# Kernel optimization log

Hardware: AMD Instinct MI355X
Metric: run time of the kernel (lower is better)

Reference implementation:

```python
import jax, jax.numpy as jnp
import numpy as np

N_GROUPS = 8
N_TOPK_GROUP = 4
TOPK = 8
ROUTED_SCALE = 2.5


def setup_inputs() -> dict:
    key = jax.random.key(0)
    k1, k2, k3 = jax.random.split(key, 3)
    T, D, E = 8192, 7168, 256
    x = jax.random.normal(k1, (T, D), dtype=jnp.float32)
    weight = jax.random.normal(k2, (E, D), dtype=jnp.float32) * 0.02
    bias = jax.random.normal(k3, (E,), dtype=jnp.float32) * 0.02
    return {"x": x, "weight": weight, "bias": bias}


def reference(x, weight, bias):
    T = x.shape[0]
    # gate projection + sigmoid -> routing scores [T, E]
    scores = jax.nn.sigmoid(jnp.einsum("td,ed->te", x, weight))
    original_scores = scores
    s = scores + bias
    # grouped top-k routing: [T, G, E/G]
    sg = s.reshape(T, N_GROUPS, -1)
    # group score = sum of top-2 expert scores within each group
    group_scores = jax.lax.top_k(sg, 2)[0].sum(axis=-1)        # [T, G]
    _, gidx = jax.lax.top_k(group_scores, N_TOPK_GROUP)        # [T, n_topk_group]
    keep = jnp.zeros((T, N_GROUPS), dtype=bool)
    keep = keep.at[jnp.arange(T)[:, None], gidx].set(True)
    sg = jnp.where(keep[:, :, None], sg, -jnp.inf)
    s = sg.reshape(T, -1)
    # per-token top-k experts over surviving groups
    _, indices = jax.lax.top_k(s, TOPK)                        # [T, topk]
    weights = jnp.take_along_axis(original_scores, indices, axis=1)
    weights = weights / weights.sum(axis=-1, keepdims=True) * ROUTED_SCALE
    return weights.astype(x.dtype), indices
```

## Files before the change

### kernel.cpp

```cpp
#include <hip/hip_runtime.h>
#include <hip/hip_bf16.h>
#include <math.h>


typedef _Float16 f16x8 __attribute__((ext_vector_type(8)));
typedef float    f32x4 __attribute__((ext_vector_type(4)));

__device__ __forceinline__ void glds16(const void* g, void* l) {
  __builtin_amdgcn_global_load_lds(
      (const __attribute__((address_space(1))) void*)g,
      (__attribute__((address_space(3))) void*)l, 16, 0, 0);
}

__device__ __forceinline__ unsigned short f2h(float f) {
  _Float16 h = (_Float16)f;
  return __builtin_bit_cast(unsigned short, h);
}
__device__ __forceinline__ float h2f(unsigned short b) {
  return (float)__builtin_bit_cast(_Float16, b);
}

__device__ __forceinline__ int swz(int gi, int row) {
  return gi ^ (row & 3) ^ ((row >> 2) & 3);
}

__global__ __launch_bounds__(256) void convert_w(
    const float* __restrict__ W,
    unsigned short* __restrict__ Whi, unsigned short* __restrict__ Wlo)
{
  const int e = blockIdx.x;
  const int t = threadIdx.x;
  if (t >= 224) return;
  const int r = e & 127, bn = e >> 7;
  const float* src = W + (size_t)e * 7168 + t * 32;
  const size_t tbase = (size_t)(bn * 224 + t) * 4096 + (size_t)r * 32;
  #pragma unroll
  for (int g = 0; g < 4; ++g) {
    unsigned int hw[4], lw[4];
    #pragma unroll
    for (int p = 0; p < 4; ++p) {
      float f0 = src[g * 8 + 2 * p] * 64.0f;
      float f1 = src[g * 8 + 2 * p + 1] * 64.0f;
      unsigned short h0 = f2h(f0), h1 = f2h(f1);
      unsigned short l0 = f2h((f0 - h2f(h0)) * 2048.0f);
      unsigned short l1 = f2h((f1 - h2f(h1)) * 2048.0f);
      hw[p] = (unsigned)h0 | ((unsigned)h1 << 16);
      lw[p] = (unsigned)l0 | ((unsigned)l1 << 16);
    }
    const size_t base = tbase + (size_t)(swz(g, r) * 8);
    *(uint4*)(Whi + base) = make_uint4(hw[0], hw[1], hw[2], hw[3]);
    *(uint4*)(Wlo + base) = make_uint4(lw[0], lw[1], lw[2], lw[3]);
  }
}

__global__ __launch_bounds__(256, 2) void gate_gemm(
    const float* __restrict__ X,
    const unsigned short* __restrict__ Whi,
    const unsigned short* __restrict__ Wlo,
    float* __restrict__ Spart, int D, int TILES, int KS)
{
  __shared__ char lds[65536];

  const int bid = blockIdx.x;
  const int ks = bid % KS;
  const int bn = (bid / KS) & 1;
  const int bm = bid / (2 * KS);
  const int tid = threadIdx.x, lane = tid & 63, wid = tid >> 6;
  const int wm = wid >> 1, wn = wid & 1;
  const int TM = bm * 128;
  const int k0base = ks * TILES * 32;

  const int srow = tid >> 1, skq = tid & 1;
  const float* xsrc = X + (size_t)(TM + srow) * D + k0base + skq * 16;
  const int aw0 = srow * 64 + swz(skq * 2 + 0, srow) * 16;
  const int aw1 = srow * 64 + swz(skq * 2 + 1, srow) * 16;

  const unsigned short* wh_tile = Whi + (size_t)(bn * 224 + ks * TILES) * 4096;
  const unsigned short* wl_tile = Wlo + (size_t)(bn * 224 + ks * TILES) * 4096;

  f32x4 acc1[4][4], acc2[4][4];
  #pragma unroll
  for (int m = 0; m < 4; ++m)
    #pragma unroll
    for (int n = 0; n < 4; ++n) { acc1[m][n] = (f32x4)0.0f; acc2[m][n] = (f32x4)0.0f; }

  int aro[4], bro[4];
  const int gi = lane >> 4;
  #pragma unroll
  for (int m = 0; m < 4; ++m) {
    const int row = wm * 64 + m * 16 + (lane & 15);
    aro[m] = row * 64 + swz(gi, row) * 16;
  }
  #pragma unroll
  for (int n = 0; n < 4; ++n) {
    const int row = wn * 64 + n * 16 + (lane & 15);
    bro[n] = row * 64 + swz(gi, row) * 16;
  }

  float4 pa[4], pb[4];
  {
    #pragma unroll
    for (int i = 0; i < 2; ++i) {
      const int c = wid * 2 + i;
      glds16(wh_tile + c * 512 + lane * 8, lds + 16384 + c * 1024);
      glds16(wl_tile + c * 512 + lane * 8, lds + 24576 + c * 1024);
    }
    __builtin_amdgcn_sched_barrier(0);
    float4 a[4];
    #pragma unroll
    for (int i = 0; i < 4; ++i) a[i] = *(const float4*)(xsrc + i * 4);
    unsigned int hw[8], lw[8];
    #pragma unroll
    for (int q = 0; q < 8; ++q) {
      float f0 = ((const float*)a)[2 * q], f1 = ((const float*)a)[2 * q + 1];
      unsigned short h0 = f2h(f0), h1 = f2h(f1);
      unsigned short l0 = f2h((f0 - h2f(h0)) * 2048.0f);
      unsigned short l1 = f2h((f1 - h2f(h1)) * 2048.0f);
      hw[q] = (unsigned)h0 | ((unsigned)h1 << 16);
      lw[q] = (unsigned)l0 | ((unsigned)l1 << 16);
    }
    *(uint4*)(lds + aw0)        = make_uint4(hw[0], hw[1], hw[2], hw[3]);
    *(uint4*)(lds + aw1)        = make_uint4(hw[4], hw[5], hw[6], hw[7]);
    *(uint4*)(lds + 8192 + aw0) = make_uint4(lw[0], lw[1], lw[2], lw[3]);
    *(uint4*)(lds + 8192 + aw1) = make_uint4(lw[4], lw[5], lw[6], lw[7]);
    const int s1 = (TILES > 1) ? 1 : 0;
    #pragma unroll
    for (int i = 0; i < 4; ++i)
      pa[i] = *(const float4*)(xsrc + (size_t)s1 * 32 + i * 4);
    __builtin_amdgcn_sched_barrier(0);
  }
  asm volatile("s_waitcnt vmcnt(4) lgkmcnt(0)" ::: "memory");
  __builtin_amdgcn_sched_barrier(0);
  __builtin_amdgcn_s_barrier();

  int cur = 0;
  for (int s = 0; s < TILES; ++s) {
    const int nxt = cur ^ 1;
    char* base_c = lds + cur * 32768;
    char* base_n = lds + nxt * 32768;
    const bool stage_next = (s + 1 < TILES);

    if (stage_next) {
      const unsigned short* wh = wh_tile + (size_t)(s + 1) * 4096;
      const unsigned short* wl = wl_tile + (size_t)(s + 1) * 4096;
      #pragma unroll
      for (int i = 0; i < 2; ++i) {
        const int c = wid * 2 + i;
        glds16(wh + c * 512 + lane * 8, base_n + 16384 + c * 1024);
        glds16(wl + c * 512 + lane * 8, base_n + 24576 + c * 1024);
      }
    }
    __builtin_amdgcn_sched_barrier(0);

    {
      int sn = s + 2; if (sn > TILES - 1) sn = TILES - 1;
      #pragma unroll
      for (int i = 0; i < 4; ++i)
        pb[i] = *(const float4*)(xsrc + (size_t)sn * 32 + i * 4);
    }
    __builtin_amdgcn_sched_barrier(0);

    {
      const char* Ahi = base_c;          const char* Alo = base_c + 8192;
      const char* Bh  = base_c + 16384;  const char* Bl  = base_c + 24576;
      f16x8 ah[4], al[4], bh[4], bl[4];
      #pragma unroll
      for (int m = 0; m < 4; ++m) {
        ah[m] = *(const f16x8*)(Ahi + aro[m]);
        al[m] = *(const f16x8*)(Alo + aro[m]);
      }
      #pragma unroll
      for (int n = 0; n < 4; ++n) {
        bh[n] = *(const f16x8*)(Bh + bro[n]);
        bl[n] = *(const f16x8*)(Bl + bro[n]);
      }
      __builtin_amdgcn_s_setprio(1);
      #pragma unroll
      for (int m = 0; m < 4; ++m)
        #pragma unroll
        for (int n = 0; n < 4; ++n) {
          acc1[m][n] = __builtin_amdgcn_mfma_f32_16x16x32_f16(ah[m], bh[n], acc1[m][n], 0, 0, 0);
          acc2[m][n] = __builtin_amdgcn_mfma_f32_16x16x32_f16(ah[m], bl[n], acc2[m][n], 0, 0, 0);
          acc2[m][n] = __builtin_amdgcn_mfma_f32_16x16x32_f16(al[m], bh[n], acc2[m][n], 0, 0, 0);
        }
      __builtin_amdgcn_s_setprio(0);
    }

    if (stage_next) {
      unsigned int hw[8], lw[8];
      #pragma unroll
      for (int q = 0; q < 8; ++q) {
        float f0 = ((const float*)pa)[2 * q], f1 = ((const float*)pa)[2 * q + 1];
        unsigned short h0 = f2h(f0), h1 = f2h(f1);
        unsigned short l0 = f2h((f0 - h2f(h0)) * 2048.0f);
        unsigned short l1 = f2h((f1 - h2f(h1)) * 2048.0f);
        hw[q] = (unsigned)h0 | ((unsigned)h1 << 16);
        lw[q] = (unsigned)l0 | ((unsigned)l1 << 16);
      }
      *(uint4*)(base_n + aw0)        = make_uint4(hw[0], hw[1], hw[2], hw[3]);
      *(uint4*)(base_n + aw1)        = make_uint4(hw[4], hw[5], hw[6], hw[7]);
      *(uint4*)(base_n + 8192 + aw0) = make_uint4(lw[0], lw[1], lw[2], lw[3]);
      *(uint4*)(base_n + 8192 + aw1) = make_uint4(lw[4], lw[5], lw[6], lw[7]);
    }
    #pragma unroll
    for (int i = 0; i < 4; ++i) pa[i] = pb[i];

    asm volatile("s_waitcnt vmcnt(4) lgkmcnt(0)" ::: "memory");
    __builtin_amdgcn_sched_barrier(0);
    __builtin_amdgcn_s_barrier();

    cur = nxt;
  }

  float* Sp = Spart + (size_t)ks * 8192 * 256;
  #pragma unroll
  for (int m = 0; m < 4; ++m)
    #pragma unroll
    for (int n = 0; n < 4; ++n)
      #pragma unroll
      for (int r = 0; r < 4; ++r) {
        const int t = TM + wm * 64 + m * 16 + (lane >> 4) * 4 + r;
        const int e = bn * 128 + wn * 64 + n * 16 + (lane & 15);
        Sp[(size_t)t * 256 + e] =
            (acc1[m][n][r] + acc2[m][n][r] * (1.0f / 2048.0f)) * (1.0f / 64.0f);
      }
}

__global__ __launch_bounds__(256) void gate_routing(
    const float* __restrict__ Spart, int KS,
    const float* __restrict__ bias,
    float* __restrict__ outw, float* __restrict__ outi, int T)
{
  const int lane = threadIdx.x & 63;
  const int wave = threadIdx.x >> 6;
  const int t = blockIdx.x * 4 + wave;
  if (t >= T) return;

  double l[4] = {0.0, 0.0, 0.0, 0.0};
  for (int ks = 0; ks < KS; ++ks) {
    float4 p = *(const float4*)(Spart + (size_t)ks * T * 256
                                + (size_t)t * 256 + lane * 4);
    l[0] += (double)p.x; l[1] += (double)p.y;
    l[2] += (double)p.z; l[3] += (double)p.w;
  }

  float4 bi = *(const float4*)(bias + lane * 4);
  float orig[4], s[4];
  #pragma unroll
  for (int u = 0; u < 4; ++u)
    orig[u] = 1.0f / (1.0f + expf(-(float)l[u]));
  s[0] = orig[0] + bi.x; s[1] = orig[1] + bi.y;
  s[2] = orig[2] + bi.z; s[3] = orig[3] + bi.w;

  float m1 = -INFINITY, m2 = -INFINITY;
  #pragma unroll
  for (int u = 0; u < 4; ++u) {
    float v = s[u];
    if (v > m1) { m2 = m1; m1 = v; }
    else if (v > m2) { m2 = v; }
  }
  #pragma unroll
  for (int off = 1; off < 8; off <<= 1) {
    float o1 = __shfl_xor(m1, off, 64);
    float o2 = __shfl_xor(m2, off, 64);
    if (o1 > m1) { m2 = fmaxf(m1, o2); m1 = o1; }
    else         { m2 = fmaxf(m2, o1); }
  }
  const float gscore = m1 + m2;

  const int g = lane >> 3;
  int rank = 0;
  #pragma unroll
  for (int j = 0; j < 8; ++j) {
    float gs = __shfl(gscore, j * 8, 64);
    rank += (gs > gscore || (gs == gscore && j < g)) ? 1 : 0;
  }
  if (rank >= 4) { s[0] = s[1] = s[2] = s[3] = -INFINITY; }

  float wsum = 0.0f, sel_w = 0.0f;
  int sel_i = 0;
  #pragma unroll
  for (int it = 0; it < 8; ++it) {
    float bv = s[0]; int bu = 0;
    #pragma unroll
    for (int u = 1; u < 4; ++u)
      if (s[u] > bv) { bv = s[u]; bu = u; }
    float v = bv;
    int ix = lane * 4 + bu;
    float og = orig[bu];
    #pragma unroll
    for (int off = 1; off < 64; off <<= 1) {
      float ov  = __shfl_xor(v,  off, 64);
      int   oix = __shfl_xor(ix, off, 64);
      float oog = __shfl_xor(og, off, 64);
      if (ov > v || (ov == v && oix < ix)) { v = ov; ix = oix; og = oog; }
    }
    if (lane == it) { sel_w = og; sel_i = ix; }
    wsum += og;
    if ((ix >> 2) == lane) s[ix & 3] = -INFINITY;
  }

  if (lane < 8) {
    outw[(size_t)t * 8 + lane] = sel_w / wsum * 2.5f;
    outi[(size_t)t * 8 + lane] = (float)sel_i;
  }
}

extern "C" void kernel_launch(void* const* d_in, const int* in_sizes, int n_in,
                              void* d_out, int out_size, void* d_ws, size_t ws_size,
                              hipStream_t stream) {
  const float* x = (const float*)d_in[0];
  const float* w = (const float*)d_in[1];
  const float* b = (const float*)d_in[2];
  const int E = in_sizes[2];
  const int D = in_sizes[1] / E;
  const int T = in_sizes[0] / D;

  unsigned short* Whi = (unsigned short*)d_ws;
  unsigned short* Wlo = (unsigned short*)((char*)d_ws + (4u << 20));
  float* Spart = (float*)((char*)d_ws + (8u << 20));

  const size_t per_part = (size_t)T * E * 4;
  int KS = 2;
  if (ws_size >= (8u << 20) + 8 * per_part) KS = 8;
  else if (ws_size >= (8u << 20) + 4 * per_part) KS = 4;
  const int TILES = D / (32 * KS);

  float* outw = (float*)d_out;
  float* outi = outw + (size_t)T * 8;

  convert_w<<<E, 256, 0, stream>>>(w, Whi, Wlo);
  gate_gemm<<<2 * KS * (T / 128), 256, 0, stream>>>(x, Whi, Wlo, Spart, D, TILES, KS);
  gate_routing<<<(T + 3) / 4, 256, 0, stream>>>(Spart, KS, b, outw, outi, T);
}
```

Measured before the change: 147.4 us.

## Split main loop into four sub-phases interleaving loads, staging and MFMA

Restructures each K-tile iteration into four phases, one per N sub-block. Each phase loads one B fragment, issues part of the global prefetch or the fp32-to-split-fp16 staging, then runs that sub-block's MFMAs. The aim is to spread memory and conversion work between MFMA bursts, ping-pong style, so latency is hidden better. In exchange it adds two workgroup barriers per phase (eight per tile instead of one), which may add synchronisation overhead.

After: 155.2 us. 1.05x slower.

```diff
diff --git a/kernel.cpp b/kernel.cpp
--- a/kernel.cpp
+++ b/kernel.cpp
@@ -135,81 +135,86 @@
 
   int cur = 0;
   for (int s = 0; s < TILES; ++s) {
-    const int nxt = cur ^ 1;
     char* base_c = lds + cur * 32768;
-    char* base_n = lds + nxt * 32768;
+    char* base_n = lds + (cur ^ 1) * 32768;
     const bool stage_next = (s + 1 < TILES);
 
-    if (stage_next) {
-      const unsigned short* wh = wh_tile + (size_t)(s + 1) * 4096;
-      const unsigned short* wl = wl_tile + (size_t)(s + 1) * 4096;
-      #pragma unroll
-      for (int i = 0; i < 2; ++i) {
-        const int c = wid * 2 + i;
-        glds16(wh + c * 512 + lane * 8, base_n + 16384 + c * 1024);
-        glds16(wl + c * 512 + lane * 8, base_n + 24576 + c * 1024);
-      }
-    }
-    __builtin_amdgcn_sched_barrier(0);
-
-    {
-      int sn = s + 2; if (sn > TILES - 1) sn = TILES - 1;
-      #pragma unroll
-      for (int i = 0; i < 4; ++i)
-        pb[i] = *(const float4*)(xsrc + (size_t)sn * 32 + i * 4);
-    }
-    __builtin_amdgcn_sched_barrier(0);
-
-    {
-      const char* Ahi = base_c;          const char* Alo = base_c + 8192;
-      const char* Bh  = base_c + 16384;  const char* Bl  = base_c + 24576;
-      f16x8 ah[4], al[4], bh[4], bl[4];
+    f16x8 ah[4], al[4];
+
+    #pragma unroll
+    for (int q = 0; q < 4; ++q) {
+      if (q == 0) {
+        #pragma unroll
+        for (int m = 0; m < 4; ++m) {
+          ah[m] = *(const f16x8*)(base_c + aro[m]);
+          al[m] = *(const f16x8*)(base_c + 8192 + aro[m]);
+        }
+      }
+      f16x8 bh = *(const f16x8*)(base_c + 16384 + bro[q]);
+      f16x8 bl = *(const f16x8*)(base_c + 24576 + bro[q]);
+
+      if (q == 0 && stage_next) {
+        const unsigned short* wh = wh_tile + (size_t)(s + 1) * 4096;
+        #pragma unroll
+        for (int i = 0; i < 2; ++i) {
+          const int c = wid * 2 + i;
+          glds16(wh + c * 512 + lane * 8, base_n + 16384 + c * 1024);
+        }
+      }
+      if (q == 1 && stage_next) {
+        const unsigned short* wl = wl_tile + (size_t)(s + 1) * 4096;
+        #pragma unroll
+        for (int i = 0; i < 2; ++i) {
+          const int c = wid * 2 + i;
+          glds16(wl + c * 512 + lane * 8, base_n + 24576 + c * 1024);
+        }
+      }
+      if (q == 2) {
+        __builtin_amdgcn_sched_barrier(0);
+        int sn = s + 2; if (sn > TILES - 1) sn = TILES - 1;
+        #pragma unroll
+        for (int i = 0; i < 4; ++i)
+          pb[i] = *(const float4*)(xsrc + (size_t)sn * 32 + i * 4);
+        __builtin_amdgcn_sched_barrier(0);
+      }
+      if (q == 3 && stage_next) {
+        unsigned int hw[8], lw[8];
+        #pragma unroll
+        for (int p = 0; p < 8; ++p) {
+          float f0 = ((const float*)pa)[2 * p], f1 = ((const float*)pa)[2 * p + 1];
+          unsigned short h0 = f2h(f0), h1 = f2h(f1);
+          unsigned short l0 = f2h((f0 - h2f(h0)) * 2048.0f);
+          unsigned short l1 = f2h((f1 - h2f(h1)) * 2048.0f);
+          hw[p] = (unsigned)h0 | ((unsigned)h1 << 16);
+          lw[p] = (unsigned)l0 | ((unsigned)l1 << 16);
+        }
+        *(uint4*)(base_n + aw0)        = make_uint4(hw[0], hw[1], hw[2], hw[3]);
+        *(uint4*)(base_n + aw1)        = make_uint4(hw[4], hw[5], hw[6], hw[7]);
+        *(uint4*)(base_n + 8192 + aw0) = make_uint4(lw[0], lw[1], lw[2], lw[3]);
+        *(uint4*)(base_n + 8192 + aw1) = make_uint4(lw[4], lw[5], lw[6], lw[7]);
+      }
+
+      __builtin_amdgcn_s_barrier();
+      asm volatile("s_waitcnt lgkmcnt(0)" ::: "memory");
+      __builtin_amdgcn_sched_barrier(0);
+      __builtin_amdgcn_s_setprio(1);
       #pragma unroll
       for (int m = 0; m < 4; ++m) {
-        ah[m] = *(const f16x8*)(Ahi + aro[m]);
-        al[m] = *(const f16x8*)(Alo + aro[m]);
-      }
-      #pragma unroll
-      for (int n = 0; n < 4; ++n) {
-        bh[n] = *(const f16x8*)(Bh + bro[n]);
-        bl[n] = *(const f16x8*)(Bl + bro[n]);
-      }
-      __builtin_amdgcn_s_setprio(1);
-      #pragma unroll
-      for (int m = 0; m < 4; ++m)
-        #pragma unroll
-        for (int n = 0; n < 4; ++n) {
-          acc1[m][n] = __builtin_amdgcn_mfma_f32_16x16x32_f16(ah[m], bh[n], acc1[m][n], 0, 0, 0);
-          acc2[m][n] = __builtin_amdgcn_mfma_f32_16x16x32_f16(ah[m], bl[n], acc2[m][n], 0, 0, 0);
-          acc2[m][n] = __builtin_amdgcn_mfma_f32_16x16x32_f16(al[m], bh[n], acc2[m][n], 0, 0, 0);
-        }
+        acc1[m][q] = __builtin_amdgcn_mfma_f32_16x16x32_f16(ah[m], bh, acc1[m][q], 0, 0, 0);
+        acc2[m][q] = __builtin_amdgcn_mfma_f32_16x16x32_f16(ah[m], bl, acc2[m][q], 0, 0, 0);
+        acc2[m][q] = __builtin_amdgcn_mfma_f32_16x16x32_f16(al[m], bh, acc2[m][q], 0, 0, 0);
+      }
       __builtin_amdgcn_s_setprio(0);
-    }
-
-    if (stage_next) {
-      unsigned int hw[8], lw[8];
-      #pragma unroll
-      for (int q = 0; q < 8; ++q) {
-        float f0 = ((const float*)pa)[2 * q], f1 = ((const float*)pa)[2 * q + 1];
-        unsigned short h0 = f2h(f0), h1 = f2h(f1);
-        unsigned short l0 = f2h((f0 - h2f(h0)) * 2048.0f);
-        unsigned short l1 = f2h((f1 - h2f(h1)) * 2048.0f);
-        hw[q] = (unsigned)h0 | ((unsigned)h1 << 16);
-        lw[q] = (unsigned)l0 | ((unsigned)l1 << 16);
-      }
-      *(uint4*)(base_n + aw0)        = make_uint4(hw[0], hw[1], hw[2], hw[3]);
-      *(uint4*)(base_n + aw1)        = make_uint4(hw[4], hw[5], hw[6], hw[7]);
-      *(uint4*)(base_n + 8192 + aw0) = make_uint4(lw[0], lw[1], lw[2], lw[3]);
-      *(uint4*)(base_n + 8192 + aw1) = make_uint4(lw[4], lw[5], lw[6], lw[7]);
-    }
+      if (q == 3) {
+        asm volatile("s_waitcnt vmcnt(4)" ::: "memory");
+        __builtin_amdgcn_sched_barrier(0);
+      }
+      __builtin_amdgcn_s_barrier();
+    }
+
     #pragma unroll
     for (int i = 0; i < 4; ++i) pa[i] = pb[i];
-
-    asm volatile("s_waitcnt vmcnt(4) lgkmcnt(0)" ::: "memory");
-    __builtin_amdgcn_sched_barrier(0);
-    __builtin_amdgcn_s_barrier();
-
-    cur = nxt;
+    cur ^= 1;
   }
 
   float* Sp = Spart + (size_t)ks * 8192 * 256;
```

## Split split-fp16 GEMM into hi-hi and cross-term passes with 256x256 tiles

Applied to the files above, without the earlier changes.

The fused three-MFMA gate GEMM becomes two launches of a templated kernel. The first computes only the hi*hi product, and the second computes the two cross terms and read-modify-writes them into the partial sums. Tiles grow to 256 tokens by all 256 experts with 512 threads, so the weight layout is rearranged and each X tile is converted once for all experts, not twice. The cross pass needs 128KB of dynamic LDS, which may limit occupancy, and it adds a second full pass over X plus read-modify-write traffic on Spart.

Result: slower. 186.9 us (+26.8%).

```diff
diff --git a/kernel.cpp b/kernel.cpp
--- a/kernel.cpp
+++ b/kernel.cpp
@@ -31,9 +31,8 @@
   const int e = blockIdx.x;
   const int t = threadIdx.x;
   if (t >= 224) return;
-  const int r = e & 127, bn = e >> 7;
   const float* src = W + (size_t)e * 7168 + t * 32;
-  const size_t tbase = (size_t)(bn * 224 + t) * 4096 + (size_t)r * 32;
+  const size_t tbase = (size_t)t * 8192 + (size_t)e * 32;
   #pragma unroll
   for (int g = 0; g < 4; ++g) {
     unsigned int hw[4], lw[4];
@@ -47,48 +46,52 @@
       hw[p] = (unsigned)h0 | ((unsigned)h1 << 16);
       lw[p] = (unsigned)l0 | ((unsigned)l1 << 16);
     }
-    const size_t base = tbase + (size_t)(swz(g, r) * 8);
+    const size_t base = tbase + (size_t)(swz(g, e) * 8);
     *(uint4*)(Whi + base) = make_uint4(hw[0], hw[1], hw[2], hw[3]);
     *(uint4*)(Wlo + base) = make_uint4(lw[0], lw[1], lw[2], lw[3]);
   }
 }
 
-__global__ __launch_bounds__(256, 2) void gate_gemm(
+template<int CROSS>
+__global__ __launch_bounds__(512, 2) void gate_gemm(
     const float* __restrict__ X,
     const unsigned short* __restrict__ Whi,
     const unsigned short* __restrict__ Wlo,
     float* __restrict__ Spart, int D, int TILES, int KS)
 {
-  __shared__ char lds[65536];
+  extern __shared__ char lds[];
+  const int BUF   = CROSS ? 65536 : 32768;
+  const int O_ALO = 16384;
+  const int O_BH  = CROSS ? 32768 : 16384;
+  const int O_BL  = 49152;
 
   const int bid = blockIdx.x;
   const int ks = bid % KS;
-  const int bn = (bid / KS) & 1;
-  const int bm = bid / (2 * KS);
+  const int bm = bid / KS;
   const int tid = threadIdx.x, lane = tid & 63, wid = tid >> 6;
-  const int wm = wid >> 1, wn = wid & 1;
-  const int TM = bm * 128;
-  const int k0base = ks * TILES * 32;
-
-  const int srow = tid >> 1, skq = tid & 1;
-  const float* xsrc = X + (size_t)(TM + srow) * D + k0base + skq * 16;
-  const int aw0 = srow * 64 + swz(skq * 2 + 0, srow) * 16;
-  const int aw1 = srow * 64 + swz(skq * 2 + 1, srow) * 16;
-
-  const unsigned short* wh_tile = Whi + (size_t)(bn * 224 + ks * TILES) * 4096;
-  const unsigned short* wl_tile = Wlo + (size_t)(bn * 224 + ks * TILES) * 4096;
-
-  f32x4 acc1[4][4], acc2[4][4];
-  #pragma unroll
-  for (int m = 0; m < 4; ++m)
-    #pragma unroll
-    for (int n = 0; n < 4; ++n) { acc1[m][n] = (f32x4)0.0f; acc2[m][n] = (f32x4)0.0f; }
-
-  int aro[4], bro[4];
+  const int wm = wid >> 2, wn = wid & 3;
+  const int TM = bm * 256;
+  const int k0 = ks * TILES * 32;
+
+  const int srow = tid >> 1, half = tid & 1;
+  const float* xsrc = X + (size_t)(TM + srow) * D + k0 + half * 16;
+  const int aw0 = srow * 64 + swz(half * 2 + 0, srow) * 16;
+  const int aw1 = srow * 64 + swz(half * 2 + 1, srow) * 16;
+
+  const unsigned short* wh_tile = Whi + (size_t)(ks * TILES) * 8192;
+  const unsigned short* wl_tile = Wlo + (size_t)(ks * TILES) * 8192;
+
+  f32x4 acc[8][4];
+  #pragma unroll
+  for (int m = 0; m < 8; ++m)
+    #pragma unroll
+    for (int n = 0; n < 4; ++n) acc[m][n] = (f32x4)0.0f;
+
+  int aro[8], bro[4];
   const int gi = lane >> 4;
   #pragma unroll
-  for (int m = 0; m < 4; ++m) {
-    const int row = wm * 64 + m * 16 + (lane & 15);
+  for (int m = 0; m < 8; ++m) {
+    const int row = wm * 128 + m * 16 + (lane & 15);
     aro[m] = row * 64 + swz(gi, row) * 16;
   }
   #pragma unroll
@@ -98,12 +101,13 @@
   }
 
   float4 pa[4], pb[4];
+
   {
     #pragma unroll
     for (int i = 0; i < 2; ++i) {
       const int c = wid * 2 + i;
-      glds16(wh_tile + c * 512 + lane * 8, lds + 16384 + c * 1024);
-      glds16(wl_tile + c * 512 + lane * 8, lds + 24576 + c * 1024);
+      glds16(wh_tile + c * 512 + lane * 8, lds + O_BH + c * 1024);
+      if (CROSS) glds16(wl_tile + c * 512 + lane * 8, lds + O_BL + c * 1024);
     }
     __builtin_amdgcn_sched_barrier(0);
     float4 a[4];
@@ -114,15 +118,19 @@
     for (int q = 0; q < 8; ++q) {
       float f0 = ((const float*)a)[2 * q], f1 = ((const float*)a)[2 * q + 1];
       unsigned short h0 = f2h(f0), h1 = f2h(f1);
-      unsigned short l0 = f2h((f0 - h2f(h0)) * 2048.0f);
-      unsigned short l1 = f2h((f1 - h2f(h1)) * 2048.0f);
       hw[q] = (unsigned)h0 | ((unsigned)h1 << 16);
-      lw[q] = (unsigned)l0 | ((unsigned)l1 << 16);
-    }
-    *(uint4*)(lds + aw0)        = make_uint4(hw[0], hw[1], hw[2], hw[3]);
-    *(uint4*)(lds + aw1)        = make_uint4(hw[4], hw[5], hw[6], hw[7]);
-    *(uint4*)(lds + 8192 + aw0) = make_uint4(lw[0], lw[1], lw[2], lw[3]);
-    *(uint4*)(lds + 8192 + aw1) = make_uint4(lw[4], lw[5], lw[6], lw[7]);
+      if (CROSS) {
+        unsigned short l0 = f2h((f0 - h2f(h0)) * 2048.0f);
+        unsigned short l1 = f2h((f1 - h2f(h1)) * 2048.0f);
+        lw[q] = (unsigned)l0 | ((unsigned)l1 << 16);
+      }
+    }
+    *(uint4*)(lds + aw0) = make_uint4(hw[0], hw[1], hw[2], hw[3]);
+    *(uint4*)(lds + aw1) = make_uint4(hw[4], hw[5], hw[6], hw[7]);
+    if (CROSS) {
+      *(uint4*)(lds + O_ALO + aw0) = make_uint4(lw[0], lw[1], lw[2], lw[3]);
+      *(uint4*)(lds + O_ALO + aw1) = make_uint4(lw[4], lw[5], lw[6], lw[7]);
+    }
     const int s1 = (TILES > 1) ? 1 : 0;
     #pragma unroll
     for (int i = 0; i < 4; ++i)
@@ -135,19 +143,18 @@
 
   int cur = 0;
   for (int s = 0; s < TILES; ++s) {
-    const int nxt = cur ^ 1;
-    char* base_c = lds + cur * 32768;
-    char* base_n = lds + nxt * 32768;
+    char* base_c = lds + cur * BUF;
+    char* base_n = lds + (cur ^ 1) * BUF;
     const bool stage_next = (s + 1 < TILES);
 
     if (stage_next) {
-      const unsigned short* wh = wh_tile + (size_t)(s + 1) * 4096;
-      const unsigned short* wl = wl_tile + (size_t)(s + 1) * 4096;
+      const unsigned short* wh = wh_tile + (size_t)(s + 1) * 8192;
+      const unsigned short* wl = wl_tile + (size_t)(s + 1) * 8192;
       #pragma unroll
       for (int i = 0; i < 2; ++i) {
         const int c = wid * 2 + i;
-        glds16(wh + c * 512 + lane * 8, base_n + 16384 + c * 1024);
-        glds16(wl + c * 512 + lane * 8, base_n + 24576 + c * 1024);
+        glds16(wh + c * 512 + lane * 8, base_n + O_BH + c * 1024);
+        if (CROSS) glds16(wl + c * 512 + lane * 8, base_n + O_BL + c * 1024);
       }
     }
     __builtin_amdgcn_sched_barrier(0);
@@ -161,28 +168,29 @@
     __builtin_amdgcn_sched_barrier(0);
 
     {
-      const char* Ahi = base_c;          const char* Alo = base_c + 8192;
-      const char* Bh  = base_c + 16384;  const char* Bl  = base_c + 24576;
-      f16x8 ah[4], al[4], bh[4], bl[4];
-      #pragma unroll
-      for (int m = 0; m < 4; ++m) {
-        ah[m] = *(const f16x8*)(Ahi + aro[m]);
-        al[m] = *(const f16x8*)(Alo + aro[m]);
-      }
+      f16x8 bh[4], bl[4];
       #pragma unroll
       for (int n = 0; n < 4; ++n) {
-        bh[n] = *(const f16x8*)(Bh + bro[n]);
-        bl[n] = *(const f16x8*)(Bl + bro[n]);
+        bh[n] = *(const f16x8*)(base_c + O_BH + bro[n]);
+        if (CROSS) bl[n] = *(const f16x8*)(base_c + O_BL + bro[n]);
       }
       __builtin_amdgcn_s_setprio(1);
       #pragma unroll
-      for (int m = 0; m < 4; ++m)
-        #pragma unroll
-        for (int n = 0; n < 4; ++n) {
-          acc1[m][n] = __builtin_amdgcn_mfma_f32_16x16x32_f16(ah[m], bh[n], acc1[m][n], 0, 0, 0);
-          acc2[m][n] = __builtin_amdgcn_mfma_f32_16x16x32_f16(ah[m], bl[n], acc2[m][n], 0, 0, 0);
-          acc2[m][n] = __builtin_amdgcn_mfma_f32_16x16x32_f16(al[m], bh[n], acc2[m][n], 0, 0, 0);
+      for (int m = 0; m < 8; ++m) {
+        f16x8 ah = *(const f16x8*)(base_c + aro[m]);
+        if (!CROSS) {
+          #pragma unroll
+          for (int n = 0; n < 4; ++n)
+            acc[m][n] = __builtin_amdgcn_mfma_f32_16x16x32_f16(ah, bh[n], acc[m][n], 0, 0, 0);
+        } else {
+          f16x8 al = *(const f16x8*)(base_c + O_ALO + aro[m]);
+          #pragma unroll
+          for (int n = 0; n < 4; ++n) {
+            acc[m][n] = __builtin_amdgcn_mfma_f32_16x16x32_f16(ah, bl[n], acc[m][n], 0, 0, 0);
+            acc[m][n] = __builtin_amdgcn_mfma_f32_16x16x32_f16(al, bh[n], acc[m][n], 0, 0, 0);
+          }
         }
+      }
       __builtin_amdgcn_s_setprio(0);
     }
 
@@ -192,15 +200,19 @@
       for (int q = 0; q < 8; ++q) {
         float f0 = ((const float*)pa)[2 * q], f1 = ((const float*)pa)[2 * q + 1];
         unsigned short h0 = f2h(f0), h1 = f2h(f1);
-        unsigned short l0 = f2h((f0 - h2f(h0)) * 2048.0f);
-        unsigned short l1 = f2h((f1 - h2f(h1)) * 2048.0f);
         hw[q] = (unsigned)h0 | ((unsigned)h1 << 16);
-        lw[q] = (unsigned)l0 | ((unsigned)l1 << 16);
-      }
-      *(uint4*)(base_n + aw0)        = make_uint4(hw[0], hw[1], hw[2], hw[3]);
-      *(uint4*)(base_n + aw1)        = make_uint4(hw[4], hw[5], hw[6], hw[7]);
-      *(uint4*)(base_n + 8192 + aw0) = make_uint4(lw[0], lw[1], lw[2], lw[3]);
-      *(uint4*)(base_n + 8192 + aw1) = make_uint4(lw[4], lw[5], lw[6], lw[7]);
+        if (CROSS) {
+          unsigned short l0 = f2h((f0 - h2f(h0)) * 2048.0f);
+          unsigned short l1 = f2h((f1 - h2f(h1)) * 2048.0f);
+          lw[q] = (unsigned)l0 | ((unsigned)l1 << 16);
+        }
+      }
+      *(uint4*)(base_n + aw0) = make_uint4(hw[0], hw[1], hw[2], hw[3]);
+      *(uint4*)(base_n + aw1) = make_uint4(hw[4], hw[5], hw[6], hw[7]);
+      if (CROSS) {
+        *(uint4*)(base_n + O_ALO + aw0) = make_uint4(lw[0], lw[1], lw[2], lw[3]);
+        *(uint4*)(base_n + O_ALO + aw1) = make_uint4(lw[4], lw[5], lw[6], lw[7]);
+      }
     }
     #pragma unroll
     for (int i = 0; i < 4; ++i) pa[i] = pb[i];
@@ -209,20 +221,22 @@
     __builtin_amdgcn_sched_barrier(0);
     __builtin_amdgcn_s_barrier();
 
-    cur = nxt;
+    cur ^= 1;
   }
 
   float* Sp = Spart + (size_t)ks * 8192 * 256;
   #pragma unroll
-  for (int m = 0; m < 4; ++m)
+  for (int m = 0; m < 8; ++m)
     #pragma unroll
     for (int n = 0; n < 4; ++n)
       #pragma unroll
       for (int r = 0; r < 4; ++r) {
-        const int t = TM + wm * 64 + m * 16 + (lane >> 4) * 4 + r;
-        const int e = bn * 128 + wn * 64 + n * 16 + (lane & 15);
-        Sp[(size_t)t * 256 + e] =
-            (acc1[m][n][r] + acc2[m][n][r] * (1.0f / 2048.0f)) * (1.0f / 64.0f);
+        const int t = TM + wm * 128 + m * 16 + (lane >> 4) * 4 + r;
+        const int e = wn * 64 + n * 16 + (lane & 15);
+        if (CROSS)
+          Sp[(size_t)t * 256 + e] += acc[m][n][r] * (1.0f / 2048.0f);
+        else
+          Sp[(size_t)t * 256 + e] = acc[m][n][r];
       }
 }
 
@@ -248,7 +262,7 @@
   float orig[4], s[4];
   #pragma unroll
   for (int u = 0; u < 4; ++u)
-    orig[u] = 1.0f / (1.0f + expf(-(float)l[u]));
+    orig[u] = 1.0f / (1.0f + expf(-(float)(l[u] * (1.0 / 64.0))));
   s[0] = orig[0] + bi.x; s[1] = orig[1] + bi.y;
   s[2] = orig[2] + bi.z; s[3] = orig[3] + bi.w;
 
@@ -321,15 +335,16 @@
   float* Spart = (float*)((char*)d_ws + (8u << 20));
 
   const size_t per_part = (size_t)T * E * 4;
-  int KS = 2;
+  int KS = 4;
   if (ws_size >= (8u << 20) + 8 * per_part) KS = 8;
-  else if (ws_size >= (8u << 20) + 4 * per_part) KS = 4;
   const int TILES = D / (32 * KS);
 
   float* outw = (float*)d_out;
   float* outi = outw + (size_t)T * 8;
 
   convert_w<<<E, 256, 0, stream>>>(w, Whi, Wlo);
-  gate_gemm<<<2 * KS * (T / 128), 256, 0, stream>>>(x, Whi, Wlo, Spart, D, TILES, KS);
+  const int grid = (T / 256) * KS;
+  gate_gemm<0><<<grid, 512, 65536,  stream>>>(x, Whi, Wlo, Spart, D, TILES, KS);
+  gate_gemm<1><<<grid, 512, 131072, stream>>>(x, Whi, Wlo, Spart, D, TILES, KS);
   gate_routing<<<(T + 3) / 4, 256, 0, stream>>>(Spart, KS, b, outw, outi, T);
 }
```

## Screen with single-fp16 GEMM, refine only near-tie tokens in split precision

Applied to the files above, without the earlier changes.

Replaces the three-MFMA hi/lo split GEMM with a single fp16 pass over all tokens, and adds a screening kernel that flags tokens whose top-k or group selection falls within a small margin. Only the flagged tokens are recomputed with the full split-precision GEMM and routed again. The intent is to cut MFMA work and LDS traffic roughly threefold for most tokens. In exchange the kernel relies on heuristic margins being wide enough to catch every precision-sensitive selection, and it adds atomics, extra launches and a refine pass whose size depends on the data.

Result: slower. 352.4 us (+139.1%).

```diff
diff --git a/kernel.cpp b/kernel.cpp
--- a/kernel.cpp
+++ b/kernel.cpp
@@ -2,6 +2,9 @@
 #include <hip/hip_bf16.h>
 #include <math.h>
 
+
+#define MARGIN  2.0e-3f
+#define GMARGIN 4.0e-3f
 
 typedef _Float16 f16x8 __attribute__((ext_vector_type(8)));
 typedef float    f32x4 __attribute__((ext_vector_type(4)));
@@ -11,7 +14,6 @@
       (const __attribute__((address_space(1))) void*)g,
       (__attribute__((address_space(3))) void*)l, 16, 0, 0);
 }
-
 __device__ __forceinline__ unsigned short f2h(float f) {
   _Float16 h = (_Float16)f;
   return __builtin_bit_cast(unsigned short, h);
@@ -19,18 +21,18 @@
 __device__ __forceinline__ float h2f(unsigned short b) {
   return (float)__builtin_bit_cast(_Float16, b);
 }
-
 __device__ __forceinline__ int swz(int gi, int row) {
   return gi ^ (row & 3) ^ ((row >> 2) & 3);
 }
 
 __global__ __launch_bounds__(256) void convert_w(
     const float* __restrict__ W,
-    unsigned short* __restrict__ Whi, unsigned short* __restrict__ Wlo)
+    unsigned short* __restrict__ Whi, unsigned short* __restrict__ Wlo,
+    int* __restrict__ cnt)
 {
   const int e = blockIdx.x;
   const int t = threadIdx.x;
-  if (t >= 224) return;
+  if (t >= 224) { if (e == 0 && t == 224) *cnt = 0; return; }
   const int r = e & 127, bn = e >> 7;
   const float* src = W + (size_t)e * 7168 + t * 32;
   const size_t tbase = (size_t)(bn * 224 + t) * 4096 + (size_t)r * 32;
@@ -53,13 +55,12 @@
   }
 }
 
-__global__ __launch_bounds__(256, 2) void gate_gemm(
+__global__ __launch_bounds__(256, 3) void gate_gemm_approx(
     const float* __restrict__ X,
     const unsigned short* __restrict__ Whi,
-    const unsigned short* __restrict__ Wlo,
     float* __restrict__ Spart, int D, int TILES, int KS)
 {
-  __shared__ char lds[65536];
+  __shared__ char lds[32768];
 
   const int bid = blockIdx.x;
   const int ks = bid % KS;
@@ -76,13 +77,12 @@
   const int aw1 = srow * 64 + swz(skq * 2 + 1, srow) * 16;
 
   const unsigned short* wh_tile = Whi + (size_t)(bn * 224 + ks * TILES) * 4096;
-  const unsigned short* wl_tile = Wlo + (size_t)(bn * 224 + ks * TILES) * 4096;
-
-  f32x4 acc1[4][4], acc2[4][4];
+
+  f32x4 acc[4][4];
   #pragma unroll
   for (int m = 0; m < 4; ++m)
     #pragma unroll
-    for (int n = 0; n < 4; ++n) { acc1[m][n] = (f32x4)0.0f; acc2[m][n] = (f32x4)0.0f; }
+    for (int n = 0; n < 4; ++n) acc[m][n] = (f32x4)0.0f;
 
   int aro[4], bro[4];
   const int gi = lane >> 4;
@@ -102,81 +102,322 @@
     #pragma unroll
     for (int i = 0; i < 2; ++i) {
       const int c = wid * 2 + i;
-      glds16(wh_tile + c * 512 + lane * 8, lds + 16384 + c * 1024);
-      glds16(wl_tile + c * 512 + lane * 8, lds + 24576 + c * 1024);
+      glds16(wh_tile + c * 512 + lane * 8, lds + 8192 + c * 1024);
     }
     __builtin_amdgcn_sched_barrier(0);
     float4 a[4];
     #pragma unroll
     for (int i = 0; i < 4; ++i) a[i] = *(const float4*)(xsrc + i * 4);
-    unsigned int hw[8], lw[8];
+    unsigned int hw[8];
     #pragma unroll
     for (int q = 0; q < 8; ++q) {
       float f0 = ((const float*)a)[2 * q], f1 = ((const float*)a)[2 * q + 1];
+      hw[q] = (unsigned)f2h(f0) | ((unsigned)f2h(f1) << 16);
+    }
+    *(uint4*)(lds + aw0) = make_uint4(hw[0], hw[1], hw[2], hw[3]);
+    *(uint4*)(lds + aw1) = make_uint4(hw[4], hw[5], hw[6], hw[7]);
+    const int s1 = (TILES > 1) ? 1 : 0;
+    #pragma unroll
+    for (int i = 0; i < 4; ++i)
+      pa[i] = *(const float4*)(xsrc + (size_t)s1 * 32 + i * 4);
+    __builtin_amdgcn_sched_barrier(0);
+  }
+  asm volatile("s_waitcnt vmcnt(4) lgkmcnt(0)" ::: "memory");
+  __builtin_amdgcn_sched_barrier(0);
+  __builtin_amdgcn_s_barrier();
+
+  int cur = 0;
+  for (int s = 0; s < TILES; ++s) {
+    char* base_c = lds + cur * 16384;
+    char* base_n = lds + (cur ^ 1) * 16384;
+    const bool stage_next = (s + 1 < TILES);
+
+    if (stage_next) {
+      const unsigned short* wh = wh_tile + (size_t)(s + 1) * 4096;
+      #pragma unroll
+      for (int i = 0; i < 2; ++i) {
+        const int c = wid * 2 + i;
+        glds16(wh + c * 512 + lane * 8, base_n + 8192 + c * 1024);
+      }
+    }
+    __builtin_amdgcn_sched_barrier(0);
+    {
+      int sn = s + 2; if (sn > TILES - 1) sn = TILES - 1;
+      #pragma unroll
+      for (int i = 0; i < 4; ++i)
+        pb[i] = *(const float4*)(xsrc + (size_t)sn * 32 + i * 4);
+    }
+    __builtin_amdgcn_sched_barrier(0);
+    {
+      f16x8 ah[4], bh[4];
+      #pragma unroll
+      for (int m = 0; m < 4; ++m) ah[m] = *(const f16x8*)(base_c + aro[m]);
+      #pragma unroll
+      for (int n = 0; n < 4; ++n) bh[n] = *(const f16x8*)(base_c + 8192 + bro[n]);
+      __builtin_amdgcn_s_setprio(1);
+      #pragma unroll
+      for (int m = 0; m < 4; ++m)
+        #pragma unroll
+        for (int n = 0; n < 4; ++n)
+          acc[m][n] = __builtin_amdgcn_mfma_f32_16x16x32_f16(ah[m], bh[n], acc[m][n], 0, 0, 0);
+      __builtin_amdgcn_s_setprio(0);
+    }
+    if (stage_next) {
+      unsigned int hw[8];
+      #pragma unroll
+      for (int q = 0; q < 8; ++q) {
+        float f0 = ((const float*)pa)[2 * q], f1 = ((const float*)pa)[2 * q + 1];
+        hw[q] = (unsigned)f2h(f0) | ((unsigned)f2h(f1) << 16);
+      }
+      *(uint4*)(base_n + aw0) = make_uint4(hw[0], hw[1], hw[2], hw[3]);
+      *(uint4*)(base_n + aw1) = make_uint4(hw[4], hw[5], hw[6], hw[7]);
+    }
+    #pragma unroll
+    for (int i = 0; i < 4; ++i) pa[i] = pb[i];
+
+    asm volatile("s_waitcnt vmcnt(4) lgkmcnt(0)" ::: "memory");
+    __builtin_amdgcn_sched_barrier(0);
+    __builtin_amdgcn_s_barrier();
+    cur ^= 1;
+  }
+
+  float* Sp = Spart + (size_t)ks * 8192 * 256;
+  #pragma unroll
+  for (int m = 0; m < 4; ++m)
+    #pragma unroll
+    for (int n = 0; n < 4; ++n)
+      #pragma unroll
+      for (int r = 0; r < 4; ++r) {
+        const int t = TM + wm * 64 + m * 16 + (lane >> 4) * 4 + r;
+        const int e = bn * 128 + wn * 64 + n * 16 + (lane & 15);
+        Sp[(size_t)t * 256 + e] = acc[m][n][r] * (1.0f / 64.0f);
+      }
+}
+
+__global__ __launch_bounds__(256) void gate_screen(
+    const float* __restrict__ Spart, int KS,
+    const float* __restrict__ bias,
+    float* __restrict__ outw, float* __restrict__ outi, int T,
+    int* __restrict__ cnt, int* __restrict__ list)
+{
+  const int lane = threadIdx.x & 63;
+  const int wave = threadIdx.x >> 6;
+  const int t = blockIdx.x * 4 + wave;
+  if (t >= T) return;
+
+  double l[4] = {0.0, 0.0, 0.0, 0.0};
+  for (int ks = 0; ks < KS; ++ks) {
+    float4 p = *(const float4*)(Spart + (size_t)ks * T * 256
+                                + (size_t)t * 256 + lane * 4);
+    l[0] += (double)p.x; l[1] += (double)p.y;
+    l[2] += (double)p.z; l[3] += (double)p.w;
+  }
+
+  float4 bi = *(const float4*)(bias + lane * 4);
+  float orig[4], s[4];
+  #pragma unroll
+  for (int u = 0; u < 4; ++u)
+    orig[u] = 1.0f / (1.0f + expf(-(float)l[u]));
+  s[0] = orig[0] + bi.x; s[1] = orig[1] + bi.y;
+  s[2] = orig[2] + bi.z; s[3] = orig[3] + bi.w;
+
+  float m1 = -INFINITY, m2 = -INFINITY;
+  #pragma unroll
+  for (int u = 0; u < 4; ++u) {
+    float v = s[u];
+    if (v > m1) { m2 = m1; m1 = v; }
+    else if (v > m2) { m2 = v; }
+  }
+  #pragma unroll
+  for (int off = 1; off < 8; off <<= 1) {
+    float o1 = __shfl_xor(m1, off, 64);
+    float o2 = __shfl_xor(m2, off, 64);
+    if (o1 > m1) { m2 = fmaxf(m1, o2); m1 = o1; }
+    else         { m2 = fmaxf(m2, o1); }
+  }
+  const float gscore = m1 + m2;
+
+  const int g = lane >> 3;
+  int rank = 0;
+  float g4 = -INFINITY, g5 = -INFINITY;
+  #pragma unroll
+  for (int j = 0; j < 8; ++j) {
+    float gs = __shfl(gscore, j * 8, 64);
+    rank += (gs > gscore || (gs == gscore && j < g)) ? 1 : 0;
+    int rj = 0;
+    #pragma unroll
+    for (int jj = 0; jj < 8; ++jj) {
+      float gjj = __shfl(gscore, jj * 8, 64);
+      rj += (gjj > gs || (gjj == gs && jj < j)) ? 1 : 0;
+    }
+    if (rj == 3) g4 = gs;
+    if (rj == 4) g5 = gs;
+  }
+  if (rank >= 4) { s[0] = s[1] = s[2] = s[3] = -INFINITY; }
+
+  float wsum = 0.0f, sel_w = 0.0f;
+  int sel_i = 0;
+  float prev_v = 0.0f, gapmin = INFINITY;
+  for (int it = 0; it < 9; ++it) {
+    float bv = s[0]; int bu = 0;
+    #pragma unroll
+    for (int u = 1; u < 4; ++u)
+      if (s[u] > bv) { bv = s[u]; bu = u; }
+    float v = bv;
+    int ix = lane * 4 + bu;
+    float og = orig[bu];
+    #pragma unroll
+    for (int off = 1; off < 64; off <<= 1) {
+      float ov  = __shfl_xor(v,  off, 64);
+      int   oix = __shfl_xor(ix, off, 64);
+      float oog = __shfl_xor(og, off, 64);
+      if (ov > v || (ov == v && oix < ix)) { v = ov; ix = oix; og = oog; }
+    }
+    if (it > 0) gapmin = fminf(gapmin, prev_v - v);
+    prev_v = v;
+    if (it < 8) {
+      if (lane == it) { sel_w = og; sel_i = ix; }
+      wsum += og;
+      if ((ix >> 2) == lane) s[ix & 3] = -INFINITY;
+    }
+  }
+
+  if (lane < 8) {
+    outw[(size_t)t * 8 + lane] = sel_w / wsum * 2.5f;
+    outi[(size_t)t * 8 + lane] = (float)sel_i;
+  }
+
+  const bool flag = (g4 - g5 < GMARGIN) || (gapmin < MARGIN);
+  if (flag && lane == 0) {
+    int pos = atomicAdd(cnt, 1);
+    list[pos] = t;
+  }
+}
+
+__global__ __launch_bounds__(256, 2) void gate_refine_gemm(
+    const float* __restrict__ X,
+    const unsigned short* __restrict__ Whi,
+    const unsigned short* __restrict__ Wlo,
+    float* __restrict__ Rpart, int D, int TILES, int KS,
+    const int* __restrict__ cnt, const int* __restrict__ list)
+{
+  const int count = *cnt;
+  const int bid = blockIdx.x;
+  const int ks = bid % KS;
+  const int bm = bid / KS;
+  if (bm * 32 >= count) return;
+
+  __shared__ char lds[73728];
+
+  const int tid = threadIdx.x, lane = tid & 63, wid = tid >> 6;
+  const int k0base = ks * TILES * 32;
+
+  const int srow = tid >> 3, sub = tid & 7;
+  const int sgi = sub >> 1, shalf = sub & 1;
+  int slot = bm * 32 + srow;
+  int sl = slot < count ? slot : count - 1;
+  const int tok = list[sl];
+  const float* xsrc = X + (size_t)tok * D + k0base + sub * 4;
+  const int aw = srow * 64 + swz(sgi, srow) * 16 + shalf * 8;
+
+  const unsigned short* wh_t0 = Whi + (size_t)(ks * TILES) * 4096;
+  const unsigned short* wh_t1 = Whi + (size_t)(224 + ks * TILES) * 4096;
+  const unsigned short* wl_t0 = Wlo + (size_t)(ks * TILES) * 4096;
+  const unsigned short* wl_t1 = Wlo + (size_t)(224 + ks * TILES) * 4096;
+
+  f32x4 acc1[2][4], acc2[2][4];
+  #pragma unroll
+  for (int m = 0; m < 2; ++m)
+    #pragma unroll
+    for (int n = 0; n < 4; ++n) { acc1[m][n] = (f32x4)0.0f; acc2[m][n] = (f32x4)0.0f; }
+
+  int aro[2], bro[4];
+  const int gi = lane >> 4;
+  #pragma unroll
+  for (int m = 0; m < 2; ++m) {
+    const int row = m * 16 + (lane & 15);
+    aro[m] = row * 64 + swz(gi, row) * 16;
+  }
+  #pragma unroll
+  for (int n = 0; n < 4; ++n) {
+    const int row = wid * 64 + n * 16 + (lane & 15);
+    bro[n] = row * 64 + swz(gi, row) * 16;
+  }
+
+  float4 pa, pb;
+  {
+    #pragma unroll
+    for (int i = 0; i < 4; ++i) {
+      const int c = wid * 4 + i;
+      const unsigned short* sh = (c < 8) ? (wh_t0 + (c & 7) * 512)
+                                         : (wh_t1 + (c & 7) * 512);
+      const unsigned short* slo = (c < 8) ? (wl_t0 + (c & 7) * 512)
+                                          : (wl_t1 + (c & 7) * 512);
+      glds16(sh + lane * 8, lds + 4096 + c * 1024);
+      glds16(slo + lane * 8, lds + 20480 + c * 1024);
+    }
+    __builtin_amdgcn_sched_barrier(0);
+    float4 a = *(const float4*)(xsrc);
+    unsigned int hw[2], lw[2];
+    const float ff[4] = {a.x, a.y, a.z, a.w};
+    #pragma unroll
+    for (int q = 0; q < 2; ++q) {
+      float f0 = ff[2 * q], f1 = ff[2 * q + 1];
       unsigned short h0 = f2h(f0), h1 = f2h(f1);
       unsigned short l0 = f2h((f0 - h2f(h0)) * 2048.0f);
       unsigned short l1 = f2h((f1 - h2f(h1)) * 2048.0f);
       hw[q] = (unsigned)h0 | ((unsigned)h1 << 16);
       lw[q] = (unsigned)l0 | ((unsigned)l1 << 16);
     }
-    *(uint4*)(lds + aw0)        = make_uint4(hw[0], hw[1], hw[2], hw[3]);
-    *(uint4*)(lds + aw1)        = make_uint4(hw[4], hw[5], hw[6], hw[7]);
-    *(uint4*)(lds + 8192 + aw0) = make_uint4(lw[0], lw[1], lw[2], lw[3]);
-    *(uint4*)(lds + 8192 + aw1) = make_uint4(lw[4], lw[5], lw[6], lw[7]);
+    *(uint2*)(lds + aw)        = make_uint2(hw[0], hw[1]);
+    *(uint2*)(lds + 2048 + aw) = make_uint2(lw[0], lw[1]);
     const int s1 = (TILES > 1) ? 1 : 0;
-    #pragma unroll
-    for (int i = 0; i < 4; ++i)
-      pa[i] = *(const float4*)(xsrc + (size_t)s1 * 32 + i * 4);
-    __builtin_amdgcn_sched_barrier(0);
-  }
-  asm volatile("s_waitcnt vmcnt(4) lgkmcnt(0)" ::: "memory");
+    pa = *(const float4*)(xsrc + (size_t)s1 * 32);
+    __builtin_amdgcn_sched_barrier(0);
+  }
+  asm volatile("s_waitcnt vmcnt(1) lgkmcnt(0)" ::: "memory");
   __builtin_amdgcn_sched_barrier(0);
   __builtin_amdgcn_s_barrier();
 
   int cur = 0;
   for (int s = 0; s < TILES; ++s) {
-    const int nxt = cur ^ 1;
-    char* base_c = lds + cur * 32768;
-    char* base_n = lds + nxt * 32768;
+    char* base_c = lds + cur * 36864;
+    char* base_n = lds + (cur ^ 1) * 36864;
     const bool stage_next = (s + 1 < TILES);
 
     if (stage_next) {
-      const unsigned short* wh = wh_tile + (size_t)(s + 1) * 4096;
-      const unsigned short* wl = wl_tile + (size_t)(s + 1) * 4096;
-      #pragma unroll
-      for (int i = 0; i < 2; ++i) {
-        const int c = wid * 2 + i;
-        glds16(wh + c * 512 + lane * 8, base_n + 16384 + c * 1024);
-        glds16(wl + c * 512 + lane * 8, base_n + 24576 + c * 1024);
-      }
-    }
-    __builtin_amdgcn_sched_barrier(0);
-
+      #pragma unroll
+      for (int i = 0; i < 4; ++i) {
+        const int c = wid * 4 + i;
+        const unsigned short* sh = ((c < 8) ? wh_t0 : wh_t1)
+                                   + (size_t)(s + 1) * 4096 + (c & 7) * 512;
+        const unsigned short* slo = ((c < 8) ? wl_t0 : wl_t1)
+                                    + (size_t)(s + 1) * 4096 + (c & 7) * 512;
+        glds16(sh + lane * 8, base_n + 4096 + c * 1024);
+        glds16(slo + lane * 8, base_n + 20480 + c * 1024);
+      }
+    }
+    __builtin_amdgcn_sched_barrier(0);
     {
       int sn = s + 2; if (sn > TILES - 1) sn = TILES - 1;
-      #pragma unroll
-      for (int i = 0; i < 4; ++i)
-        pb[i] = *(const float4*)(xsrc + (size_t)sn * 32 + i * 4);
-    }
-    __builtin_amdgcn_sched_barrier(0);
-
+      pb = *(const float4*)(xsrc + (size_t)sn * 32);
+    }
+    __builtin_amdgcn_sched_barrier(0);
     {
-      const char* Ahi = base_c;          const char* Alo = base_c + 8192;
-      const char* Bh  = base_c + 16384;  const char* Bl  = base_c + 24576;
-      f16x8 ah[4], al[4], bh[4], bl[4];
-      #pragma unroll
-      for (int m = 0; m < 4; ++m) {
-        ah[m] = *(const f16x8*)(Ahi + aro[m]);
-        al[m] = *(const f16x8*)(Alo + aro[m]);
+      f16x8 ah[2], al[2], bh[4], bl[4];
+      #pragma unroll
+      for (int m = 0; m < 2; ++m) {
+        ah[m] = *(const f16x8*)(base_c + aro[m]);
+        al[m] = *(const f16x8*)(base_c + 2048 + aro[m]);
       }
       #pragma unroll
       for (int n = 0; n < 4; ++n) {
-        bh[n] = *(const f16x8*)(Bh + bro[n]);
-        bl[n] = *(const f16x8*)(Bl + bro[n]);
+        bh[n] = *(const f16x8*)(base_c + 4096 + bro[n]);
+        bl[n] = *(const f16x8*)(base_c + 20480 + bro[n]);
       }
       __builtin_amdgcn_s_setprio(1);
       #pragma unroll
-      for (int m = 0; m < 4; ++m)
+      for (int m = 0; m < 2; ++m)
         #pragma unroll
         for (int n = 0; n < 4; ++n) {
           acc1[m][n] = __builtin_amdgcn_mfma_f32_16x16x32_f16(ah[m], bh[n], acc1[m][n], 0, 0, 0);
@@ -185,61 +426,59 @@
         }
       __builtin_amdgcn_s_setprio(0);
     }
-
     if (stage_next) {
-      unsigned int hw[8], lw[8];
-      #pragma unroll
-      for (int q = 0; q < 8; ++q) {
-        float f0 = ((const float*)pa)[2 * q], f1 = ((const float*)pa)[2 * q + 1];
+      unsigned int hw[2], lw[2];
+      const float ff[4] = {pa.x, pa.y, pa.z, pa.w};
+      #pragma unroll
+      for (int q = 0; q < 2; ++q) {
+        float f0 = ff[2 * q], f1 = ff[2 * q + 1];
         unsigned short h0 = f2h(f0), h1 = f2h(f1);
         unsigned short l0 = f2h((f0 - h2f(h0)) * 2048.0f);
         unsigned short l1 = f2h((f1 - h2f(h1)) * 2048.0f);
         hw[q] = (unsigned)h0 | ((unsigned)h1 << 16);
         lw[q] = (unsigned)l0 | ((unsigned)l1 << 16);
       }
-      *(uint4*)(base_n + aw0)        = make_uint4(hw[0], hw[1], hw[2], hw[3]);
-      *(uint4*)(base_n + aw1)        = make_uint4(hw[4], hw[5], hw[6], hw[7]);
-      *(uint4*)(base_n + 8192 + aw0) = make_uint4(lw[0], lw[1], lw[2], lw[3]);
-      *(uint4*)(base_n + 8192 + aw1) = make_uint4(lw[4], lw[5], lw[6], lw[7]);
-    }
-    #pragma unroll
-    for (int i = 0; i < 4; ++i) pa[i] = pb[i];
-
-    asm volatile("s_waitcnt vmcnt(4) lgkmcnt(0)" ::: "memory");
+      *(uint2*)(base_n + aw)        = make_uint2(hw[0], hw[1]);
+      *(uint2*)(base_n + 2048 + aw) = make_uint2(lw[0], lw[1]);
+    }
+    pa = pb;
+
+    asm volatile("s_waitcnt vmcnt(1) lgkmcnt(0)" ::: "memory");
     __builtin_amdgcn_sched_barrier(0);
     __builtin_amdgcn_s_barrier();
-
-    cur = nxt;
-  }
-
-  float* Sp = Spart + (size_t)ks * 8192 * 256;
-  #pragma unroll
-  for (int m = 0; m < 4; ++m)
+    cur ^= 1;
+  }
+
+  float* Rp = Rpart + (size_t)ks * 8192 * 256;
+  #pragma unroll
+  for (int m = 0; m < 2; ++m)
     #pragma unroll
     for (int n = 0; n < 4; ++n)
       #pragma unroll
       for (int r = 0; r < 4; ++r) {
-        const int t = TM + wm * 64 + m * 16 + (lane >> 4) * 4 + r;
-        const int e = bn * 128 + wn * 64 + n * 16 + (lane & 15);
-        Sp[(size_t)t * 256 + e] =
+        const int so = bm * 32 + m * 16 + (lane >> 4) * 4 + r;
+        const int e = wid * 64 + n * 16 + (lane & 15);
+        Rp[(size_t)so * 256 + e] =
             (acc1[m][n][r] + acc2[m][n][r] * (1.0f / 2048.0f)) * (1.0f / 64.0f);
       }
 }
 
-__global__ __launch_bounds__(256) void gate_routing(
-    const float* __restrict__ Spart, int KS,
+__global__ __launch_bounds__(256) void gate_refine_route(
+    const float* __restrict__ Rpart, int KS,
     const float* __restrict__ bias,
-    float* __restrict__ outw, float* __restrict__ outi, int T)
+    float* __restrict__ outw, float* __restrict__ outi, int T,
+    const int* __restrict__ cnt, const int* __restrict__ list)
 {
   const int lane = threadIdx.x & 63;
   const int wave = threadIdx.x >> 6;
-  const int t = blockIdx.x * 4 + wave;
-  if (t >= T) return;
+  const int slot = blockIdx.x * 4 + wave;
+  if (slot >= *cnt) return;
+  const int t = list[slot];
 
   double l[4] = {0.0, 0.0, 0.0, 0.0};
   for (int ks = 0; ks < KS; ++ks) {
-    float4 p = *(const float4*)(Spart + (size_t)ks * T * 256
-                                + (size_t)t * 256 + lane * 4);
+    float4 p = *(const float4*)(Rpart + (size_t)ks * T * 256
+                                + (size_t)slot * 256 + lane * 4);
     l[0] += (double)p.x; l[1] += (double)p.y;
     l[2] += (double)p.z; l[3] += (double)p.w;
   }
@@ -316,20 +555,29 @@
   const int D = in_sizes[1] / E;
   const int T = in_sizes[0] / D;
 
+  const size_t per_part = (size_t)T * E * 4;
+  int KS = 4;
+  if (ws_size >= (8u << 20) + 8 * per_part + (1u << 20)) KS = 8;
+  const int TILES = D / (32 * KS);
+
   unsigned short* Whi = (unsigned short*)d_ws;
   unsigned short* Wlo = (unsigned short*)((char*)d_ws + (4u << 20));
   float* Spart = (float*)((char*)d_ws + (8u << 20));
-
-  const size_t per_part = (size_t)T * E * 4;
-  int KS = 2;
-  if (ws_size >= (8u << 20) + 8 * per_part) KS = 8;
-  else if (ws_size >= (8u << 20) + 4 * per_part) KS = 4;
-  const int TILES = D / (32 * KS);
+  float* Rpart = Spart;
+  char*  tail  = (char*)d_ws + (8u << 20) + (size_t)KS * per_part;
+  int*   cnt   = (int*)tail;
+  int*   list  = (int*)(tail + 1024);
 
   float* outw = (float*)d_out;
   float* outi = outw + (size_t)T * 8;
 
-  convert_w<<<E, 256, 0, stream>>>(w, Whi, Wlo);
-  gate_gemm<<<2 * KS * (T / 128), 256, 0, stream>>>(x, Whi, Wlo, Spart, D, TILES, KS);
-  gate_routing<<<(T + 3) / 4, 256, 0, stream>>>(Spart, KS, b, outw, outi, T);
-}
+  convert_w<<<E, 256, 0, stream>>>(w, Whi, Wlo, cnt);
+  gate_gemm_approx<<<2 * KS * (T / 128), 256, 0, stream>>>(
+      x, Whi, Spart, D, TILES, KS);
+  gate_screen<<<(T + 3) / 4, 256, 0, stream>>>(
+      Spart, KS, b, outw, outi, T, cnt, list);
+  gate_refine_gemm<<<(T / 32) * KS, 256, 0, stream>>>(
+      x, Whi, Wlo, Rpart, D, TILES, KS, cnt, list);
+  gate_refine_route<<<(T + 3) / 4, 256, 0, stream>>>(
+      Rpart, KS, b, outw, outi, T, cnt, list);
+}
```
